# Kernel tuning notes

Measured on AMD Instinct MI355X. Metric: run time of the kernel, lower is better.

The kernel has to match this reference:

```python
import jax, jax.numpy as jnp
import numpy as np

DIM = 1024
NUM_HEADS = 16
HEAD_DIM = DIM // NUM_HEADS
B, S = 2, 2048


def setup_inputs() -> dict:
    key = jax.random.key(0)
    k1, k2, k3 = jax.random.split(key, 3)
    x = jax.random.normal(k1, (B, S, DIM), dtype=jnp.float32)
    # torch Linear stores weight [out,in]; we store transposed [in,out] for x @ W
    w_qkv = jax.random.normal(k2, (DIM, 3 * DIM), dtype=jnp.float32) * (DIM ** -0.5)
    b_qkv = jnp.zeros((3 * DIM,), dtype=jnp.float32)
    w_proj = jax.random.normal(k3, (DIM, DIM), dtype=jnp.float32) * (DIM ** -0.5)
    b_proj = jnp.zeros((DIM,), dtype=jnp.float32)
    return {"x": x, "w_qkv": w_qkv, "b_qkv": b_qkv, "w_proj": w_proj, "b_proj": b_proj}


def reference(x, w_qkv, b_qkv, w_proj, b_proj):
    b, s, d = x.shape
    h = HEAD_DIM
    qkv = x @ w_qkv + b_qkv                              # [b,s,3d]
    qkv = qkv.reshape(b, s, 3, NUM_HEADS, h)
    q = jnp.transpose(qkv[:, :, 0], (0, 2, 1, 3))        # [b,nh,s,h]
    k = jnp.transpose(qkv[:, :, 1], (0, 2, 1, 3))
    v = jnp.transpose(qkv[:, :, 2], (0, 2, 1, 3))
    scores = jnp.einsum("bnqh,bnkh->bnqk", q, k) * (h ** -0.5)  # [b,nh,s,s]
    attn = jax.nn.softmax(scores, axis=-1)               # attn_drop is identity (p=0)
    out = jnp.einsum("bnqk,bnkh->bnqh", attn, v)         # [b,nh,s,h]
    out = jnp.transpose(out, (0, 2, 1, 3)).reshape(b, s, d)
    out = out @ w_proj + b_proj                          # proj_drop is identity (p=0)
    return out
```

## Files before the change

### kernel.cpp

```cpp
#include <hip/hip_runtime.h>
#include <hip/hip_bf16.h>

#define DIM    1024
#define NHEADS 16
#define HDIM   64
#define BB     2
#define SS     2048
#define MTOT   (BB * SS)

typedef unsigned short u16;
typedef __attribute__((ext_vector_type(8))) short short8;
typedef __attribute__((ext_vector_type(4))) float f32x4;

__device__ inline u16 f2b(float f) {
  __hip_bfloat16 h = __float2bfloat16(f);
  return *reinterpret_cast<u16*>(&h);
}
__device__ inline f32x4 zero4() { f32x4 v = {0.f, 0.f, 0.f, 0.f}; return v; }

#define GLD_LDS16(GP, LP)                                                   \
  __builtin_amdgcn_global_load_lds(                                         \
      (const __attribute__((address_space(1))) unsigned int*)               \
          (unsigned long long)(const void*)(GP),                            \
      (__attribute__((address_space(3))) unsigned int*)                     \
          (unsigned int)(unsigned long long)(const void*)(LP),              \
      16, 0, 0)

#define QSCALE 0.18033688011112042f

__global__ __launch_bounds__(256) void prep_kernel(
    const float* __restrict__ x, const float* __restrict__ wq,
    const float* __restrict__ wp,
    u16* __restrict__ x_bf, u16* __restrict__ wqt, u16* __restrict__ wpt) {
  __shared__ u16 tile[32][36];
  const int t   = threadIdx.x;
  const int blk = blockIdx.x;
  if (blk < 2048) {
    const int i = blk * 256 + t;
    const float4 a = ((const float4*)x)[i * 2];
    const float4 b = ((const float4*)x)[i * 2 + 1];
    union { u16 u[8]; uint4 v; } r;
    r.u[0] = f2b(a.x); r.u[1] = f2b(a.y); r.u[2] = f2b(a.z); r.u[3] = f2b(a.w);
    r.u[4] = f2b(b.x); r.u[5] = f2b(b.y); r.u[6] = f2b(b.z); r.u[7] = f2b(b.w);
    ((uint4*)x_bf)[i] = r.v;
    return;
  }
  const float* __restrict__ in;
  u16* __restrict__ out;
  int N, n0, k0;
  if (blk < 5120) {
    const int b2 = blk - 2048;
    in = wq; out = wqt; N = 3072;
    n0 = (b2 % 96) * 32; k0 = (b2 / 96) * 32;
  } else {
    const int b2 = blk - 5120;
    in = wp; out = wpt; N = 1024;
    n0 = (b2 & 31) * 32; k0 = (b2 >> 5) * 32;
  }
  const int tr = t >> 3, tc4 = (t & 7) * 4;
  const float4 a = *(const float4*)&in[(size_t)(k0 + tr) * N + n0 + tc4];
  tile[tr][tc4 + 0] = f2b(a.x); tile[tr][tc4 + 1] = f2b(a.y);
  tile[tr][tc4 + 2] = f2b(a.z); tile[tr][tc4 + 3] = f2b(a.w);
  __syncthreads();
  union { u16 u[4]; uint2 v; } pk;
  pk.u[0] = tile[tc4 + 0][tr]; pk.u[1] = tile[tc4 + 1][tr];
  pk.u[2] = tile[tc4 + 2][tr]; pk.u[3] = tile[tc4 + 3][tr];
  *(uint2*)&out[(size_t)(n0 + tr) * DIM + k0 + tc4] = pk.v;
}

__global__ __launch_bounds__(256) void gemm_qkv_bf16(
    const u16* __restrict__ xa, const u16* __restrict__ wt,
    const float* __restrict__ bias,
    u16* __restrict__ qbuf, u16* __restrict__ kbuf, u16* __restrict__ vtbuf) {
  __shared__ __align__(16) u16 As[128 * 64];
  __shared__ __align__(16) u16 Bs[128 * 64];
  const int tid = threadIdx.x, w = tid >> 6, lane = tid & 63;
  const int l15 = lane & 15, l4 = lane >> 4;
  const int lin = blockIdx.x;
  const int swz = (lin & 7) * 96 + (lin >> 3);
  const int m0 = (swz & 31) * 128, n0 = (swz >> 5) * 128;
  const int wm = (w >> 1) * 64, wn = (w & 1) * 64;

  f32x4 acc[4][4];
#pragma unroll
  for (int i = 0; i < 4; ++i)
#pragma unroll
    for (int j = 0; j < 4; ++j) acc[i][j] = zero4();

  for (int k0 = 0; k0 < DIM; k0 += 64) {
#pragma unroll
    for (int j = 0; j < 4; ++j) {
      const int rowX = (w * 4 + j) * 8 + (lane >> 3);
      const int kcol = k0 + (lane & 7) * 8;
      GLD_LDS16(&xa[(size_t)(m0 + rowX) * DIM + kcol], &As[(w * 4 + j) * 512]);
      GLD_LDS16(&wt[(size_t)(n0 + rowX) * DIM + kcol], &Bs[(w * 4 + j) * 512]);
    }
    asm volatile("s_waitcnt vmcnt(0)" ::: "memory");
    __syncthreads();
#pragma unroll
    for (int kc = 0; kc < 2; ++kc) {
      short8 af[4], bfr[4];
#pragma unroll
      for (int mb = 0; mb < 4; ++mb)
        af[mb] = *(const short8*)&As[(wm + mb * 16 + l15) * 64 + kc * 32 + l4 * 8];
#pragma unroll
      for (int nb = 0; nb < 4; ++nb)
        bfr[nb] = *(const short8*)&Bs[(wn + nb * 16 + l15) * 64 + kc * 32 + l4 * 8];
#pragma unroll
      for (int mb = 0; mb < 4; ++mb)
#pragma unroll
        for (int nb = 0; nb < 4; ++nb)
          acc[mb][nb] = __builtin_amdgcn_mfma_f32_16x16x32_bf16(
              af[mb], bfr[nb], acc[mb][nb], 0, 0, 0);
    }
    __syncthreads();
  }

  const int colb  = n0 + wn;
  const int which = colb >> 10;
  const int head  = (colb & 1023) >> 6;
  if (which == 2) {
    u16* __restrict__ wl = ((w < 2) ? As : Bs) + (w & 1) * 4096;
    const int rowbase = m0 + wm;
    const int bidx = rowbase >> 11, sbase = rowbase & 2047;
    float bv[4];
#pragma unroll
    for (int nb = 0; nb < 4; ++nb) bv[nb] = bias[colb + nb * 16 + l15];
#pragma unroll
    for (int nb = 0; nb < 4; ++nb) {
      const int h = nb * 16 + l15;
#pragma unroll
      for (int mb = 0; mb < 4; ++mb) {
        union { u16 u[4]; uint2 v; } pk;
#pragma unroll
        for (int r = 0; r < 4; ++r) pk.u[r] = f2b(acc[mb][nb][r] + bv[nb]);
        const int csw = (mb * 2 + (l4 >> 1)) ^ (l15 & 7);
        *(uint2*)&wl[h * 64 + csw * 8 + (l4 & 1) * 4] = pk.v;
      }
    }
#pragma unroll
    for (int p = 0; p < 8; ++p) {
      const int h = (lane >> 3) + p * 8;
      const int csw = (lane & 7) ^ (h & 7);
      const uint4 d = *(const uint4*)&wl[h * 64 + csw * 8];
      *(uint4*)&vtbuf[((size_t)((bidx * NHEADS + head) * 64 + h)) * SS +
                      sbase + (lane & 7) * 8] = d;
    }
  } else {
    u16* __restrict__ dst = (which == 0) ? qbuf : kbuf;
    const float scale = (which == 0) ? QSCALE : 1.0f;
#pragma unroll
    for (int nb = 0; nb < 4; ++nb) {
      const int col = colb + nb * 16 + l15;
      const float bv = bias[col];
      const int h = col & 63;
#pragma unroll
      for (int mb = 0; mb < 4; ++mb)
#pragma unroll
        for (int r = 0; r < 4; ++r) {
          const int row = m0 + wm + mb * 16 + l4 * 4 + r;
          const int b = row >> 11, s = row & 2047;
          dst[((size_t)((b * NHEADS + head) * SS + s)) * 64 + h] =
              f2b((acc[mb][nb][r] + bv) * scale);
        }
    }
  }
}

__global__ __launch_bounds__(512, 4) void attn_mfma(
    const u16* __restrict__ qbuf, const u16* __restrict__ kbuf,
    const u16* __restrict__ vtbuf, u16* __restrict__ aobuf) {
  __shared__ __align__(16) u16 Ks[2][64 * 64];
  __shared__ __align__(16) u16 Vs[3 * 64 * 64];
  __shared__ __align__(16) u16 Ps[8][16 * 64];
  const int tid = threadIdx.x, w = tid >> 6, lane = tid & 63;
  const int l15 = lane & 15, l4 = lane >> 4;
  const int lin = blockIdx.x;
  const int swz = (lin & 7) * 64 + (lin >> 3);
  const int bh = swz >> 4, qt = swz & 15;
  const int b = bh >> 4, head = bh & 15;

  const u16* __restrict__ qsrc  = qbuf + ((size_t)(bh * SS + qt * 128 + w * 16)) * 64;
  const u16* __restrict__ kbase = kbuf + (size_t)bh * SS * 64;
  const u16* __restrict__ vtb   = vtbuf + (size_t)bh * 64 * SS;

  short8 qf[2];
#pragma unroll
  for (int kc = 0; kc < 2; ++kc)
    qf[kc] = *(const short8*)&qsrc[l15 * 64 + kc * 32 + l4 * 8];

  const int srow  = w * 8 + (lane >> 3);
  const int schk  = (lane & 7) ^ (srow & 7);

#define STAGEK(t, bi)                                                         \
  GLD_LDS16(kbase + ((size_t)((t) * 64 + srow)) * 64 + schk * 8,              \
            &Ks[bi][w * 8 * 64]);
#define STAGEV(t, vi)                                                         \
  GLD_LDS16(vtb + (size_t)srow * SS + (t) * 64 + schk * 8,                    \
            &Vs[(vi) * 4096 + w * 8 * 64]);

#define QKT(KB, sc)                                                           \
  {                                                                           \
    _Pragma("unroll") for (int i = 0; i < 4; ++i) sc[i] = zero4();            \
    __builtin_amdgcn_s_setprio(1);                                            \
    _Pragma("unroll") for (int kc = 0; kc < 2; ++kc)                          \
      _Pragma("unroll") for (int nb = 0; nb < 4; ++nb) {                      \
        const int key = nb * 16 + l15;                                        \
        const int cc = (kc * 4 + l4) ^ (l15 & 7);                             \
        const short8 kf = *(const short8*)&(KB)[key * 64 + cc * 8];           \
        sc[nb] = __builtin_amdgcn_mfma_f32_16x16x32_bf16(kf, qf[kc], sc[nb],  \
                                                          0, 0, 0);           \
      }                                                                       \
    __builtin_amdgcn_s_setprio(0);                                            \
  }

#define SOFTMAX_P(sc)                                                         \
  {                                                                           \
    float t0 = fmaxf(fmaxf(sc[0][0], sc[0][1]), sc[0][2]);                    \
    t0 = fmaxf(fmaxf(t0, sc[0][3]), sc[1][0]);                                \
    t0 = fmaxf(fmaxf(t0, sc[1][1]), sc[1][2]);                                \
    t0 = fmaxf(fmaxf(t0, sc[1][3]), sc[2][0]);                                \
    t0 = fmaxf(fmaxf(t0, sc[2][1]), sc[2][2]);                                \
    t0 = fmaxf(fmaxf(t0, sc[2][3]), sc[3][0]);                                \
    t0 = fmaxf(fmaxf(t0, sc[3][1]), sc[3][2]);                                \
    float tmax = fmaxf(t0, sc[3][3]);                                         \
    tmax = fmaxf(tmax, __shfl_xor(tmax, 16));                                 \
    tmax = fmaxf(tmax, __shfl_xor(tmax, 32));                                 \
    if (__ballot(tmax > mrun + 8.0f)) {                                       \
      const float mnew = fmaxf(mrun, tmax);                                   \
      const float f = exp2f(mrun - mnew);                                     \
      mrun = mnew;                                                            \
      lrun *= f;                                                              \
      _Pragma("unroll") for (int nb = 0; nb < 4; ++nb)                        \
        _Pragma("unroll") for (int r = 0; r < 4; ++r) acco[nb][r] *= f;       \
    }                                                                         \
    float p[4][4], rs = 0.f;                                                  \
    _Pragma("unroll") for (int nb = 0; nb < 4; ++nb)                          \
      _Pragma("unroll") for (int r = 0; r < 4; ++r) {                         \
        p[nb][r] = exp2f(sc[nb][r] - mrun);                                   \
        rs += p[nb][r];                                                       \
      }                                                                       \
    rs += __shfl_xor(rs, 16);                                                 \
    rs += __shfl_xor(rs, 32);                                                 \
    lrun += rs;                                                               \
    _Pragma("unroll") for (int nb = 0; nb < 4; ++nb) {                        \
      union { u16 u[4]; uint2 v; } pk;                                        \
      _Pragma("unroll") for (int r = 0; r < 4; ++r) pk.u[r] = f2b(p[nb][r]);  \
      const int cc = (nb * 2 + (l4 >> 1)) ^ (l15 & 7);                        \
      *(uint2*)&Ps[w][l15 * 64 + cc * 8 + (l4 & 1) * 4] = pk.v;               \
    }                                                                         \
  }

#define PVSTEP(vi)                                                            \
  {                                                                           \
    __builtin_amdgcn_s_setprio(1);                                            \
    _Pragma("unroll") for (int kc = 0; kc < 2; ++kc) {                        \
      const int ccp = (kc * 4 + l4) ^ (l15 & 7);                              \
      const short8 pf = *(const short8*)&Ps[w][l15 * 64 + ccp * 8];           \
      _Pragma("unroll") for (int nb = 0; nb < 4; ++nb) {                      \
        const int h = nb * 16 + l15;                                          \
        const int cv = (kc * 4 + l4) ^ (l15 & 7);                             \
        const short8 vf =                                                     \
            *(const short8*)&Vs[(vi) * 4096 + h * 64 + cv * 8];               \
        acco[nb] = __builtin_amdgcn_mfma_f32_16x16x32_bf16(vf, pf, acco[nb],  \
                                                            0, 0, 0);         \
      }                                                                       \
    }                                                                         \
    __builtin_amdgcn_s_setprio(0);                                            \
  }

  STAGEK(0, 0); STAGEV(0, 0);
  asm volatile("s_waitcnt vmcnt(0)" ::: "memory");
  __syncthreads();

  f32x4 acco[4];
#pragma unroll
  for (int i = 0; i < 4; ++i) acco[i] = zero4();
  float mrun = -1e30f, lrun = 0.f;

  f32x4 scA[4], scB[4];
  QKT(Ks[0], scA);
  STAGEK(1, 1); STAGEV(1, 1);

  int va = 0, vb = 1, vc = 2;
  for (int t2 = 0; t2 < 16; ++t2) {
    const int t = 2 * t2;
    asm volatile("s_waitcnt vmcnt(0)" ::: "memory");
    __syncthreads();
    QKT(Ks[1], scB);
    if (t + 2 < 32) { STAGEK(t + 2, 0); STAGEV(t + 2, vc); }
    SOFTMAX_P(scA);
    PVSTEP(va);
    if (t2 < 15) {
      asm volatile("s_waitcnt vmcnt(0)" ::: "memory");
      __syncthreads();
      QKT(Ks[0], scA);
      STAGEK(t + 3, 1); STAGEV(t + 3, va);
      SOFTMAX_P(scB);
      PVSTEP(vb);
      const int ova = va, ovb = vb;
      va = vc; vb = ova; vc = ovb;
    } else {
      SOFTMAX_P(scB);
      PVSTEP(vb);
    }
  }
#undef STAGEK
#undef STAGEV
#undef QKT
#undef SOFTMAX_P
#undef PVSTEP

  const float inv = 1.f / lrun;
  const int s = qt * 128 + w * 16 + l15;
  u16* __restrict__ dst = aobuf + (size_t)(b * SS + s) * DIM + head * 64;
#pragma unroll
  for (int nb = 0; nb < 4; ++nb) {
    union { u16 u[4]; uint2 v; } pk;
#pragma unroll
    for (int r = 0; r < 4; ++r) pk.u[r] = f2b(acco[nb][r] * inv);
    *(uint2*)&dst[nb * 16 + l4 * 4] = pk.v;
  }
}

__global__ __launch_bounds__(256) void gemm_proj_bf16(
    const u16* __restrict__ ao, const u16* __restrict__ wpt,
    const float* __restrict__ bias, float* __restrict__ out) {
  __shared__ __align__(16) u16 As[128 * 64];
  __shared__ __align__(16) u16 Bs[64 * 64];
  const int tid = threadIdx.x, w = tid >> 6, lane = tid & 63;
  const int l15 = lane & 15, l4 = lane >> 4;
  const int lin = blockIdx.x;
  const int swz = (lin & 7) * 64 + (lin >> 3);
  const int m0 = (swz & 31) * 128, n0 = (swz >> 5) * 64;
  const int wm = (w >> 1) * 64, wn = (w & 1) * 32;

  f32x4 acc[4][2];
#pragma unroll
  for (int i = 0; i < 4; ++i)
#pragma unroll
    for (int j = 0; j < 2; ++j) acc[i][j] = zero4();

  for (int k0 = 0; k0 < DIM; k0 += 64) {
#pragma unroll
    for (int j = 0; j < 4; ++j) {
      const int rowA = (w * 4 + j) * 8 + (lane >> 3);
      GLD_LDS16(&ao[(size_t)(m0 + rowA) * DIM + k0 + (lane & 7) * 8],
                &As[(w * 4 + j) * 512]);
    }
#pragma unroll
    for (int j = 0; j < 2; ++j) {
      const int rowB = (w * 2 + j) * 8 + (lane >> 3);
      GLD_LDS16(&wpt[(size_t)(n0 + rowB) * DIM + k0 + (lane & 7) * 8],
                &Bs[(w * 2 + j) * 512]);
    }
    asm volatile("s_waitcnt vmcnt(0)" ::: "memory");
    __syncthreads();
#pragma unroll
    for (int kc = 0; kc < 2; ++kc) {
      short8 af[4], bfr[2];
#pragma unroll
      for (int mb = 0; mb < 4; ++mb)
        af[mb] = *(const short8*)&As[(wm + mb * 16 + l15) * 64 + kc * 32 + l4 * 8];
#pragma unroll
      for (int nb = 0; nb < 2; ++nb)
        bfr[nb] = *(const short8*)&Bs[(wn + nb * 16 + l15) * 64 + kc * 32 + l4 * 8];
#pragma unroll
      for (int mb = 0; mb < 4; ++mb)
#pragma unroll
        for (int nb = 0; nb < 2; ++nb)
          acc[mb][nb] = __builtin_amdgcn_mfma_f32_16x16x32_bf16(
              af[mb], bfr[nb], acc[mb][nb], 0, 0, 0);
    }
    __syncthreads();
  }
#pragma unroll
  for (int nb = 0; nb < 2; ++nb) {
    const int col = n0 + wn + nb * 16 + l15;
    const float bv = bias[col];
#pragma unroll
    for (int mb = 0; mb < 4; ++mb)
#pragma unroll
      for (int r = 0; r < 4; ++r) {
        const int row = m0 + wm + mb * 16 + l4 * 4 + r;
        out[(size_t)row * DIM + col] = acc[mb][nb][r] + bv;
      }
  }
}

extern "C" void kernel_launch(void* const* d_in, const int* in_sizes, int n_in,
                              void* d_out, int out_size, void* d_ws, size_t ws_size,
                              hipStream_t stream) {
  const float* x      = (const float*)d_in[0];
  const float* w_qkv  = (const float*)d_in[1];
  const float* b_qkv  = (const float*)d_in[2];
  const float* w_proj = (const float*)d_in[3];
  const float* b_proj = (const float*)d_in[4];
  float* out = (float*)d_out;

  u16* ws = (u16*)d_ws;
  u16* x_bf    = ws;
  u16* wqkv_t  = x_bf   + (size_t)MTOT * DIM;
  u16* wproj_t = wqkv_t + (size_t)3 * DIM * DIM;
  u16* qbuf    = wproj_t + (size_t)DIM * DIM;
  u16* kbuf    = qbuf + (size_t)MTOT * DIM;
  u16* vtbuf   = kbuf + (size_t)MTOT * DIM;
  u16* aobuf   = x_bf;

  prep_kernel<<<6144, 256, 0, stream>>>(x, w_qkv, w_proj, x_bf, wqkv_t, wproj_t);
  gemm_qkv_bf16<<<768, 256, 0, stream>>>(x_bf, wqkv_t, b_qkv, qbuf, kbuf, vtbuf);
  attn_mfma<<<512, 512, 0, stream>>>(qbuf, kbuf, vtbuf, aobuf);
  gemm_proj_bf16<<<512, 256, 0, stream>>>(aobuf, wproj_t, b_proj, out);
}
```

Baseline: 223.8 us.

## Double-buffer LDS tiles in QKV and projection GEMMs to overlap loads

Both GEMM kernels now use two LDS buffers. The next K-tile's global-to-LDS loads are issued before the MFMA work on the current tile, and the wait on those loads moves to the end of each iteration. This is meant to hide global memory latency behind compute. LDS use per block doubles (64KB for QKV, 48KB for proj), and launch bounds gain min-blocks hints, which could reduce occupancy or constrain registers.

```diff
diff --git a/kernel.cpp b/kernel.cpp
--- a/kernel.cpp
+++ b/kernel.cpp
@@ -68,12 +68,13 @@
   *(uint2*)&out[(size_t)(n0 + tr) * DIM + k0 + tc4] = pk.v;
 }
 
-__global__ __launch_bounds__(256) void gemm_qkv_bf16(
+__global__ __launch_bounds__(256, 2) void gemm_qkv_bf16(
     const u16* __restrict__ xa, const u16* __restrict__ wt,
     const float* __restrict__ bias,
     u16* __restrict__ qbuf, u16* __restrict__ kbuf, u16* __restrict__ vtbuf) {
-  __shared__ __align__(16) u16 As[128 * 64];
-  __shared__ __align__(16) u16 Bs[128 * 64];
+  __shared__ __align__(16) u16 lds[32768];
+  u16* __restrict__ AsB = lds;
+  u16* __restrict__ BsB = lds + 16384;
   const int tid = threadIdx.x, w = tid >> 6, lane = tid & 63;
   const int l15 = lane & 15, l4 = lane >> 4;
   const int lin = blockIdx.x;
@@ -87,16 +88,25 @@
 #pragma unroll
     for (int j = 0; j < 4; ++j) acc[i][j] = zero4();
 
-  for (int k0 = 0; k0 < DIM; k0 += 64) {
-#pragma unroll
-    for (int j = 0; j < 4; ++j) {
-      const int rowX = (w * 4 + j) * 8 + (lane >> 3);
-      const int kcol = k0 + (lane & 7) * 8;
-      GLD_LDS16(&xa[(size_t)(m0 + rowX) * DIM + kcol], &As[(w * 4 + j) * 512]);
-      GLD_LDS16(&wt[(size_t)(n0 + rowX) * DIM + kcol], &Bs[(w * 4 + j) * 512]);
-    }
-    asm volatile("s_waitcnt vmcnt(0)" ::: "memory");
-    __syncthreads();
+#define STAGEG(kk, bi)                                                        \
+  _Pragma("unroll") for (int j = 0; j < 4; ++j) {                             \
+    const int rowX = (w * 4 + j) * 8 + (lane >> 3);                           \
+    const int kcol = (kk) * 64 + (lane & 7) * 8;                              \
+    GLD_LDS16(&xa[(size_t)(m0 + rowX) * DIM + kcol],                          \
+              &AsB[(bi) * 8192 + (w * 4 + j) * 512]);                         \
+    GLD_LDS16(&wt[(size_t)(n0 + rowX) * DIM + kcol],                          \
+              &BsB[(bi) * 8192 + (w * 4 + j) * 512]);                         \
+  }
+
+  STAGEG(0, 0);
+  asm volatile("s_waitcnt vmcnt(0)" ::: "memory");
+  __syncthreads();
+
+  for (int kk = 0; kk < 16; ++kk) {
+    const int cur = kk & 1;
+    if (kk + 1 < 16) STAGEG(kk + 1, 1 - cur);
+    const u16* __restrict__ As = AsB + cur * 8192;
+    const u16* __restrict__ Bs = BsB + cur * 8192;
 #pragma unroll
     for (int kc = 0; kc < 2; ++kc) {
       short8 af[4], bfr[4];
@@ -113,14 +123,16 @@
           acc[mb][nb] = __builtin_amdgcn_mfma_f32_16x16x32_bf16(
               af[mb], bfr[nb], acc[mb][nb], 0, 0, 0);
     }
+    asm volatile("s_waitcnt vmcnt(0)" ::: "memory");
     __syncthreads();
   }
+#undef STAGEG
 
   const int colb  = n0 + wn;
   const int which = colb >> 10;
   const int head  = (colb & 1023) >> 6;
   if (which == 2) {
-    u16* __restrict__ wl = ((w < 2) ? As : Bs) + (w & 1) * 4096;
+    u16* __restrict__ wl = lds + w * 4096;
     const int rowbase = m0 + wm;
     const int bidx = rowbase >> 11, sbase = rowbase & 2047;
     float bv[4];
@@ -323,11 +335,12 @@
   }
 }
 
-__global__ __launch_bounds__(256) void gemm_proj_bf16(
+__global__ __launch_bounds__(256, 3) void gemm_proj_bf16(
     const u16* __restrict__ ao, const u16* __restrict__ wpt,
     const float* __restrict__ bias, float* __restrict__ out) {
-  __shared__ __align__(16) u16 As[128 * 64];
-  __shared__ __align__(16) u16 Bs[64 * 64];
+  __shared__ __align__(16) u16 lds[24576];
+  u16* __restrict__ AsB = lds;
+  u16* __restrict__ BsB = lds + 16384;
   const int tid = threadIdx.x, w = tid >> 6, lane = tid & 63;
   const int l15 = lane & 15, l4 = lane >> 4;
   const int lin = blockIdx.x;
@@ -341,21 +354,27 @@
 #pragma unroll
     for (int j = 0; j < 2; ++j) acc[i][j] = zero4();
 
-  for (int k0 = 0; k0 < DIM; k0 += 64) {
-#pragma unroll
-    for (int j = 0; j < 4; ++j) {
-      const int rowA = (w * 4 + j) * 8 + (lane >> 3);
-      GLD_LDS16(&ao[(size_t)(m0 + rowA) * DIM + k0 + (lane & 7) * 8],
-                &As[(w * 4 + j) * 512]);
-    }
-#pragma unroll
-    for (int j = 0; j < 2; ++j) {
-      const int rowB = (w * 2 + j) * 8 + (lane >> 3);
-      GLD_LDS16(&wpt[(size_t)(n0 + rowB) * DIM + k0 + (lane & 7) * 8],
-                &Bs[(w * 2 + j) * 512]);
-    }
-    asm volatile("s_waitcnt vmcnt(0)" ::: "memory");
-    __syncthreads();
+#define STAGEP(kk, bi)                                                        \
+  _Pragma("unroll") for (int j = 0; j < 4; ++j) {                             \
+    const int rowA = (w * 4 + j) * 8 + (lane >> 3);                           \
+    GLD_LDS16(&ao[(size_t)(m0 + rowA) * DIM + (kk) * 64 + (lane & 7) * 8],    \
+              &AsB[(bi) * 8192 + (w * 4 + j) * 512]);                         \
+  }                                                                           \
+  _Pragma("unroll") for (int j = 0; j < 2; ++j) {                             \
+    const int rowB = (w * 2 + j) * 8 + (lane >> 3);                           \
+    GLD_LDS16(&wpt[(size_t)(n0 + rowB) * DIM + (kk) * 64 + (lane & 7) * 8],   \
+              &BsB[(bi) * 4096 + (w * 2 + j) * 512]);                         \
+  }
+
+  STAGEP(0, 0);
+  asm volatile("s_waitcnt vmcnt(0)" ::: "memory");
+  __syncthreads();
+
+  for (int kk = 0; kk < 16; ++kk) {
+    const int cur = kk & 1;
+    if (kk + 1 < 16) STAGEP(kk + 1, 1 - cur);
+    const u16* __restrict__ As = AsB + cur * 8192;
+    const u16* __restrict__ Bs = BsB + cur * 4096;
 #pragma unroll
     for (int kc = 0; kc < 2; ++kc) {
       short8 af[4], bfr[2];
@@ -372,8 +391,11 @@
           acc[mb][nb] = __builtin_amdgcn_mfma_f32_16x16x32_bf16(
               af[mb], bfr[nb], acc[mb][nb], 0, 0, 0);
     }
+    asm volatile("s_waitcnt vmcnt(0)" ::: "memory");
     __syncthreads();
   }
+#undef STAGEP
+
 #pragma unroll
   for (int nb = 0; nb < 2; ++nb) {
     const int col = n0 + wn + nb * 16 + l15;
```

Measured after the change: 205.1 us. 8.4% less time.
